# Optimization experiments

Measured on AMD Instinct MI355X. Metric: run time of the kernel, lower is better.

The kernel has to match this reference:

```python
import jax, jax.numpy as jnp
import numpy as np

N = 100000        # total nodes across the batch of graphs
E = 1600000       # directed edges (avg degree 16)
B = 64            # number of graphs
IN_C = 4
HID = 128


def gcn_conv(x, W, b, src, dst, n):
    """PyG GCNConv: add self-loops, symmetric deg normalization, scatter-add."""
    h = x @ W                                   # [n, out]
    loop = jnp.arange(n)
    s = jnp.concatenate([src, loop])            # [E+n] sources (with self-loops)
    d = jnp.concatenate([dst, loop])            # [E+n] targets
    deg = jax.ops.segment_sum(jnp.ones_like(s, dtype=h.dtype), d, num_segments=n)
    dinv = jnp.where(deg > 0, jax.lax.rsqrt(deg), 0.0)
    norm = dinv[s] * dinv[d]                    # [E+n]
    out = jax.ops.segment_sum(h[s] * norm[:, None], d, num_segments=n)
    return out + b


def setup_inputs() -> dict:
    key = jax.random.key(0)
    k1, k2, k3, k4, k5, k6, k7 = jax.random.split(key, 7)
    x = jax.random.normal(k1, (N, IN_C), dtype=jnp.float32)
    edge_index = jax.random.randint(k2, (2, E), 0, N, dtype=jnp.int64)
    batch = jnp.sort(jax.random.randint(k3, (N,), 0, B, dtype=jnp.int64))
    W1 = jax.random.normal(k4, (IN_C, HID), dtype=jnp.float32) / np.sqrt(IN_C)
    b1 = jnp.zeros((HID,), dtype=jnp.float32)
    W2 = jax.random.normal(k5, (HID, HID), dtype=jnp.float32) / np.sqrt(HID)
    b2 = jnp.zeros((HID,), dtype=jnp.float32)
    return {"x": x, "edge_index": edge_index, "batch": batch,
            "W1": W1, "b1": b1, "W2": W2, "b2": b2}


def reference(x, edge_index, batch, W1, b1, W2, b2):
    src, dst = edge_index[0], edge_index[1]
    n = x.shape[0]
    h = jax.nn.relu(gcn_conv(x, W1, b1, src, dst, n))
    h = jax.nn.relu(gcn_conv(h, W2, b2, src, dst, n))
    # global_mean_pool: scatter-mean by graph id
    s = jax.ops.segment_sum(h, batch, num_segments=B)                       # [B, HID]
    cnt = jax.ops.segment_sum(jnp.ones((n,), h.dtype), batch, num_segments=B)
    return s / jnp.maximum(cnt, 1.0)[:, None]
```

## Files before the change

kernel.cpp:

```cpp
#include <hip/hip_runtime.h>

#define TPB 256
#define HID 128
#define IN_C 4
#define SLOT_C 32
#define NB 512
#define EPT 8
#define ECAP 4096
#define OVF_CAP 131072

typedef __attribute__((ext_vector_type(8))) short bf16x8;
typedef __attribute__((ext_vector_type(4))) float f32x4;

union FragU { uint4 u; bf16x8 b; };

__device__ __forceinline__ unsigned f2bf(float f) {
    unsigned u = __float_as_uint(f);
    return (u + 0x7fffu + ((u >> 16) & 1u)) >> 16;
}
__device__ __forceinline__ float bf_lo(unsigned u) { return __uint_as_float(u << 16); }
__device__ __forceinline__ float bf_hi(unsigned u) { return __uint_as_float(u & 0xffff0000u); }

__global__ void k_prep(int* cursor, float* out, int n, int outsz,
                       const float* __restrict__ W2, unsigned short* w2f,
                       const int* __restrict__ batch, int* cnt, int bg,
                       int* ovf_cnt, int* pcur) {
    int nbA = (n + TPB - 1) / TPB;
    int b = blockIdx.x;
    if (b < nbA) {
        int i = b * TPB + threadIdx.x;
        if (i < n) cursor[i] = 0;
        if (i < outsz) out[i] = 0.0f;
    } else if (b < nbA + 64) {
        int i = (b - nbA) * TPB + threadIdx.x;
        if (i < HID * HID) {
            int j = i & 7, frag = i >> 3;
            int lane = frag & 63, blk = frag >> 6;
            int kk = blk >> 3, nt = blk & 7;
            int quad = lane >> 4, nloc = lane & 15;
            int k = kk * 32 + quad * 8 + j;
            int c = nt * 16 + nloc;
            w2f[i] = (unsigned short)f2bf(W2[k * HID + c]);
        }
    } else {
        int g = threadIdx.x;
        if (g == 0) *ovf_cnt = 0;
        for (int z = g; z < NB; z += TPB) pcur[z] = 0;
        if (g < bg) {
            int lo0 = 0, hi0 = n;
            while (lo0 < hi0) { int m = (lo0 + hi0) >> 1; if (batch[m] < g) lo0 = m + 1; else hi0 = m; }
            int lo1 = lo0, hi1 = n;
            while (lo1 < hi1) { int m = (lo1 + hi1) >> 1; if (batch[m] < g + 1) lo1 = m + 1; else hi1 = m; }
            cnt[g] = lo1 - lo0;
        }
    }
}

__global__ __launch_bounds__(256) void k_part(
        const int* __restrict__ src, const int* __restrict__ dst,
        int2* elist, int* pcur, int e, int n) {
    __shared__ int lcnt[2][NB];
    __shared__ int lbase[NB];
    int t = threadIdx.x;
    int c = (t >> 5) & 1;
    for (int z = t; z < NB; z += 256) { lcnt[0][z] = 0; lcnt[1][z] = 0; }
    __syncthreads();

    int base_i = blockIdx.x * (256 * EPT);
    int s[EPT], d[EPT], pr[EPT];
#pragma unroll
    for (int k = 0; k < EPT; k++) {
        int i = base_i + k * 256 + t;
        if (i < e) {
            s[k] = src[i];
            d[k] = dst[i];
            int p = (int)(((long long)d[k] * NB) / n);
            int r = atomicAdd(&lcnt[c][p], 1);
            pr[k] = p | (r << 9);
        } else {
            pr[k] = -1;
        }
    }
    __syncthreads();

    for (int z = t; z < NB; z += 256) {
        int tot = lcnt[0][z] + lcnt[1][z];
        lbase[z] = tot ? atomicAdd(&pcur[z], tot) : 0;
    }
    __syncthreads();

#pragma unroll
    for (int k = 0; k < EPT; k++) {
        if (pr[k] >= 0) {
            int p = pr[k] & (NB - 1);
            int r = pr[k] >> 9;
            int idx = lbase[p] + (c ? lcnt[0][p] : 0) + r;
            if (idx < ECAP)
                elist[(size_t)p * ECAP + idx] = make_int2(s[k], d[k]);
        }
    }
}

__global__ __launch_bounds__(256) void k_build(
        const int2* __restrict__ elist, const int* __restrict__ pcur,
        int* cursor, int* slots, int* ovf, int* ovf_cnt, int n) {
    __shared__ int lcur[512];
    int p = blockIdx.x;
    int t = threadIdx.x;
    int nlo = (int)(((long long)p * n + NB - 1) / NB);
    int nhi = (int)(((long long)(p + 1) * n + NB - 1) / NB);
    int nn = nhi - nlo;
    for (int z = t; z < nn; z += 256) lcur[z] = 0;
    __syncthreads();

    int ne = pcur[p];
    if (ne > ECAP) ne = ECAP;
    for (int j = t; j < ne; j += 256) {
        int2 ed = elist[(size_t)p * ECAP + j];
        int pos = atomicAdd(&lcur[ed.y - nlo], 1);
        if (pos < SLOT_C) {
            slots[ed.y * SLOT_C + pos] = ed.x;
        } else {
            int o = atomicAdd(ovf_cnt, 1);
            if (o < OVF_CAP) {
                ovf[2 * o] = ed.x;
                ovf[2 * o + 1] = ed.y;
            }
        }
    }
    __syncthreads();
    for (int z = t; z < nn; z += 256) cursor[nlo + z] = lcur[z];
}

__global__ void k_dinv(const int* __restrict__ cursor, float* dinv, int n) {
    int i = blockIdx.x * blockDim.x + threadIdx.x;
    if (i < n) dinv[i] = rsqrtf((float)cursor[i] + 1.0f);
}

__global__ __launch_bounds__(256) void k_g1f1(
        const int* __restrict__ cursor, const int* __restrict__ slots,
        const int* __restrict__ ovf, const int* __restrict__ ovf_cnt,
        const float* __restrict__ dinv, const float* __restrict__ x,
        const float* __restrict__ W1, const float* __restrict__ b1,
        unsigned* f1p, int n) {
    __shared__ float xs[256 * 5];
    int t = threadIdx.x;
    int v0 = blockIdx.x * 256;

    int v = v0 + t;
    if (v < n) {
        float dv = dinv[v];
        const float4* x4 = (const float4*)x;
        float4 xv = x4[v];
        float sl = dv * dv;
        float4 A = make_float4(sl * xv.x, sl * xv.y, sl * xv.z, sl * xv.w);
        float4 B = make_float4(0.f, 0.f, 0.f, 0.f);
        float4 C = make_float4(0.f, 0.f, 0.f, 0.f);
        float4 D = make_float4(0.f, 0.f, 0.f, 0.f);
        int deg = cursor[v];
        int m = deg < SLOT_C ? deg : SLOT_C;
        const int* sb = slots + v * SLOT_C;
        int e = 0;
        for (; e + 4 <= m; e += 4) {
            int s0 = sb[e], s1 = sb[e + 1], s2 = sb[e + 2], s3 = sb[e + 3];
            float n0 = dinv[s0] * dv, n1 = dinv[s1] * dv;
            float n2 = dinv[s2] * dv, n3 = dinv[s3] * dv;
            float4 r0 = x4[s0], r1 = x4[s1], r2 = x4[s2], r3 = x4[s3];
            A.x = fmaf(n0, r0.x, A.x); A.y = fmaf(n0, r0.y, A.y);
            A.z = fmaf(n0, r0.z, A.z); A.w = fmaf(n0, r0.w, A.w);
            B.x = fmaf(n1, r1.x, B.x); B.y = fmaf(n1, r1.y, B.y);
            B.z = fmaf(n1, r1.z, B.z); B.w = fmaf(n1, r1.w, B.w);
            C.x = fmaf(n2, r2.x, C.x); C.y = fmaf(n2, r2.y, C.y);
            C.z = fmaf(n2, r2.z, C.z); C.w = fmaf(n2, r2.w, C.w);
            D.x = fmaf(n3, r3.x, D.x); D.y = fmaf(n3, r3.y, D.y);
            D.z = fmaf(n3, r3.z, D.z); D.w = fmaf(n3, r3.w, D.w);
        }
        for (; e < m; e++) {
            int s = sb[e];
            float nm = dinv[s] * dv;
            float4 r = x4[s];
            A.x = fmaf(nm, r.x, A.x); A.y = fmaf(nm, r.y, A.y);
            A.z = fmaf(nm, r.z, A.z); A.w = fmaf(nm, r.w, A.w);
        }
        if (deg > SLOT_C) {
            int oc = *ovf_cnt;
            for (int k = 0; k < oc; k++) {
                if (ovf[2 * k + 1] == v) {
                    int s = ovf[2 * k];
                    float nm = dinv[s] * dv;
                    float4 r = x4[s];
                    A.x = fmaf(nm, r.x, A.x); A.y = fmaf(nm, r.y, A.y);
                    A.z = fmaf(nm, r.z, A.z); A.w = fmaf(nm, r.w, A.w);
                }
            }
        }
        xs[t * 5 + 0] = (A.x + B.x) + (C.x + D.x);
        xs[t * 5 + 1] = (A.y + B.y) + (C.y + D.y);
        xs[t * 5 + 2] = (A.z + B.z) + (C.z + D.z);
        xs[t * 5 + 3] = (A.w + B.w) + (C.w + D.w);
    }
    __syncthreads();

    int cp = t & 63;
    int c0 = cp * 2, c1 = c0 + 1;
    float w00 = W1[c0],           w01 = W1[c1];
    float w10 = W1[HID + c0],     w11 = W1[HID + c1];
    float w20 = W1[2 * HID + c0], w21 = W1[2 * HID + c1];
    float w30 = W1[3 * HID + c0], w31 = W1[3 * HID + c1];
    float bb0 = b1[c0],           bb1 = b1[c1];
    int g = t >> 6;
    for (int iter = 0; iter < 64; iter++) {
        int node = iter * 4 + g;
        int vv = v0 + node;
        if (vv >= n) break;
        float x0 = xs[node * 5 + 0], x1 = xs[node * 5 + 1];
        float x2 = xs[node * 5 + 2], x3 = xs[node * 5 + 3];
        float s0 = fmaf(x0, w00, fmaf(x1, w10, fmaf(x2, w20, fmaf(x3, w30, bb0))));
        float s1 = fmaf(x0, w01, fmaf(x1, w11, fmaf(x2, w21, fmaf(x3, w31, bb1))));
        s0 = s0 > 0.0f ? s0 : 0.0f;
        s1 = s1 > 0.0f ? s1 : 0.0f;
        f1p[(size_t)vv * 64 + cp] = f2bf(s0) | (f2bf(s1) << 16);
    }
}

__global__ __launch_bounds__(256) void k_gather2(
        const int* __restrict__ cursor, const int* __restrict__ slots,
        const int* __restrict__ ovf, const int* __restrict__ ovf_cnt,
        const float* __restrict__ dinv, const unsigned* __restrict__ f1p,
        unsigned* acc2b, int n) {
    int wv = threadIdx.x >> 6;
    int ln = threadIdx.x & 63;
    int h  = ln >> 5;
    int q  = ln & 31;
    int v = blockIdx.x * 4 + wv;
    if (v >= n) return;
    float dv = dinv[v];
    const uint2* F = (const uint2*)f1p;

    uint2 us = F[(size_t)v * 32 + q];
    float sl = (h == 0) ? dv * dv : 0.0f;
    float A[4] = { sl * bf_lo(us.x), sl * bf_hi(us.x),
                   sl * bf_lo(us.y), sl * bf_hi(us.y) };
    float B[4] = {0.f, 0.f, 0.f, 0.f};
    float C[4] = {0.f, 0.f, 0.f, 0.f};
    float D[4] = {0.f, 0.f, 0.f, 0.f};

    int deg = cursor[v];
    int m = deg < SLOT_C ? deg : SLOT_C;
    const int* sb = slots + v * SLOT_C;
    int e = 0;
    for (; e + 8 <= m; e += 8) {
        int sA = sb[e + h];
        int sB = sb[e + 2 + h];
        int sC = sb[e + 4 + h];
        int sD = sb[e + 6 + h];
        float nA = dinv[sA] * dv, nB = dinv[sB] * dv;
        float nC = dinv[sC] * dv, nD = dinv[sD] * dv;
        uint2 uA = F[(size_t)sA * 32 + q];
        uint2 uB = F[(size_t)sB * 32 + q];
        uint2 uC = F[(size_t)sC * 32 + q];
        uint2 uD = F[(size_t)sD * 32 + q];
        A[0] = fmaf(nA, bf_lo(uA.x), A[0]); A[1] = fmaf(nA, bf_hi(uA.x), A[1]);
        A[2] = fmaf(nA, bf_lo(uA.y), A[2]); A[3] = fmaf(nA, bf_hi(uA.y), A[3]);
        B[0] = fmaf(nB, bf_lo(uB.x), B[0]); B[1] = fmaf(nB, bf_hi(uB.x), B[1]);
        B[2] = fmaf(nB, bf_lo(uB.y), B[2]); B[3] = fmaf(nB, bf_hi(uB.y), B[3]);
        C[0] = fmaf(nC, bf_lo(uC.x), C[0]); C[1] = fmaf(nC, bf_hi(uC.x), C[1]);
        C[2] = fmaf(nC, bf_lo(uC.y), C[2]); C[3] = fmaf(nC, bf_hi(uC.y), C[3]);
        D[0] = fmaf(nD, bf_lo(uD.x), D[0]); D[1] = fmaf(nD, bf_hi(uD.x), D[1]);
        D[2] = fmaf(nD, bf_lo(uD.y), D[2]); D[3] = fmaf(nD, bf_hi(uD.y), D[3]);
    }
    for (; e + 2 <= m; e += 2) {
        int s = sb[e + h];
        float nm = dinv[s] * dv;
        uint2 u = F[(size_t)s * 32 + q];
        A[0] = fmaf(nm, bf_lo(u.x), A[0]); A[1] = fmaf(nm, bf_hi(u.x), A[1]);
        A[2] = fmaf(nm, bf_lo(u.y), A[2]); A[3] = fmaf(nm, bf_hi(u.y), A[3]);
    }
    if (e < m) {
        int s = sb[e];
        float nm = (h == 0) ? dinv[s] * dv : 0.0f;
        uint2 u = F[(size_t)s * 32 + q];
        A[0] = fmaf(nm, bf_lo(u.x), A[0]); A[1] = fmaf(nm, bf_hi(u.x), A[1]);
        A[2] = fmaf(nm, bf_lo(u.y), A[2]); A[3] = fmaf(nm, bf_hi(u.y), A[3]);
    }
    if (deg > SLOT_C) {
        int oc = *ovf_cnt;
        for (int k = 0; k < oc; k++) {
            if (ovf[2 * k + 1] == v && h == 0) {
                int s = ovf[2 * k];
                float nm = dinv[s] * dv;
                uint2 u = F[(size_t)s * 32 + q];
                A[0] = fmaf(nm, bf_lo(u.x), A[0]); A[1] = fmaf(nm, bf_hi(u.x), A[1]);
                A[2] = fmaf(nm, bf_lo(u.y), A[2]); A[3] = fmaf(nm, bf_hi(u.y), A[3]);
            }
        }
    }

    float o0 = (A[0] + B[0]) + (C[0] + D[0]);
    float o1 = (A[1] + B[1]) + (C[1] + D[1]);
    float o2 = (A[2] + B[2]) + (C[2] + D[2]);
    float o3 = (A[3] + B[3]) + (C[3] + D[3]);
    o0 += __shfl_xor(o0, 32, 64);
    o1 += __shfl_xor(o1, 32, 64);
    o2 += __shfl_xor(o2, 32, 64);
    o3 += __shfl_xor(o3, 32, 64);
    if (h == 0) {
        uint2 w;
        w.x = f2bf(o0) | (f2bf(o1) << 16);
        w.y = f2bf(o2) | (f2bf(o3) << 16);
        ((uint2*)acc2b)[(size_t)v * 32 + q] = w;
    }
}

__global__ __launch_bounds__(256) void k_mm2_pool(
        const unsigned* __restrict__ acc2b, const unsigned short* __restrict__ w2f,
        const float* __restrict__ b2, const int* __restrict__ batch,
        float* out, int n) {
    __shared__ int bch[64];
    int t = threadIdx.x;
    int w = t >> 6, lane = t & 63;
    int quad = lane >> 4, nloc = lane & 15;
    int v0 = blockIdx.x * 64;
    if (t < 64) {
        int v = v0 + t;
        bch[t] = (v < n) ? batch[v] : -1;
    }
    __syncthreads();

    int va = v0 + w * 16 + nloc;
    if (va >= n) va = n - 1;

    const uint4* A4 = (const uint4*)acc2b;
    const uint4* B4 = (const uint4*)w2f;

    f32x4 acc[8];
#pragma unroll
    for (int nt = 0; nt < 8; nt++) acc[nt] = (f32x4){0.f, 0.f, 0.f, 0.f};

#pragma unroll
    for (int kk = 0; kk < 4; kk++) {
        FragU af;
        af.u = A4[(size_t)va * 16 + kk * 4 + quad];
#pragma unroll
        for (int nt = 0; nt < 8; nt++) {
            FragU bf;
            bf.u = B4[(kk * 8 + nt) * 64 + lane];
            acc[nt] = __builtin_amdgcn_mfma_f32_16x16x32_bf16(af.b, bf.b, acc[nt], 0, 0, 0);
        }
    }

    int b0 = bch[w * 16], b15 = bch[w * 16 + 15];
    if (b0 == b15 && b0 >= 0) {
#pragma unroll
        for (int nt = 0; nt < 8; nt++) {
            float bias = b2[nt * 16 + nloc];
            float s = 0.f;
#pragma unroll
            for (int reg = 0; reg < 4; reg++) {
                float f = acc[nt][reg] + bias;
                s += f > 0.f ? f : 0.f;
            }
            s += __shfl_xor(s, 16, 64);
            s += __shfl_xor(s, 32, 64);
            if (lane < 16) atomicAdd(&out[b0 * HID + nt * 16 + lane], s);
        }
    } else {
#pragma unroll
        for (int nt = 0; nt < 8; nt++) {
            float bias = b2[nt * 16 + nloc];
            int cur = -1; float run = 0.f;
#pragma unroll
            for (int reg = 0; reg < 4; reg++) {
                int b = bch[w * 16 + quad * 4 + reg];
                if (b < 0) continue;
                float f = acc[nt][reg] + bias;
                f = f > 0.f ? f : 0.f;
                if (b != cur) {
                    if (cur >= 0) atomicAdd(&out[cur * HID + nt * 16 + nloc], run);
                    run = 0.f; cur = b;
                }
                run += f;
            }
            if (cur >= 0) atomicAdd(&out[cur * HID + nt * 16 + nloc], run);
        }
    }
}

__global__ void k_div(float* out, const int* __restrict__ cnt, int outsz) {
    int i = blockIdx.x * blockDim.x + threadIdx.x;
    if (i < outsz) {
        int b = i >> 7;
        float cf = (float)cnt[b];
        out[i] = out[i] / fmaxf(cf, 1.0f);
    }
}

extern "C" void kernel_launch(void* const* d_in, const int* in_sizes, int n_in,
                              void* d_out, int out_size, void* d_ws, size_t ws_size,
                              hipStream_t stream) {
    const float* x   = (const float*)d_in[0];
    const int* ei    = (const int*)d_in[1];
    const int* batch = (const int*)d_in[2];
    const float* W1  = (const float*)d_in[3];
    const float* b1  = (const float*)d_in[4];
    const float* W2  = (const float*)d_in[5];
    const float* b2  = (const float*)d_in[6];
    float* out = (float*)d_out;

    int n  = in_sizes[0] / IN_C;
    int e  = in_sizes[1] / 2;
    int bg = out_size / HID;
    const int* src = ei;
    const int* dst = ei + e;

    size_t off_b = 0;
    char* base = (char*)d_ws;
    auto carve = [&](size_t bytes) -> void* {
        void* p = base + off_b;
        off_b += (bytes + 255) & ~(size_t)255;
        return p;
    };
    int*            cursor  = (int*)carve((size_t)n * 4);
    int*            slots   = (int*)carve((size_t)n * SLOT_C * 4);
    int*            ovf     = (int*)carve((size_t)OVF_CAP * 2 * 4);
    int*            ovf_cnt = (int*)carve(256);
    int*            pcur    = (int*)carve((size_t)NB * 4);
    int2*           elist   = (int2*)carve((size_t)NB * ECAP * 8);
    float*          dinv    = (float*)carve((size_t)n * 4);
    unsigned*       f1p     = (unsigned*)carve((size_t)n * 64 * 4);
    unsigned*       acc2b   = (unsigned*)carve((size_t)n * 64 * 4);
    unsigned short* w2f     = (unsigned short*)carve((size_t)HID * HID * 2);
    int*            cnt     = (int*)carve((size_t)bg * 4);
    (void)ws_size;

    int gN = (n + TPB - 1) / TPB;
    int gP = (e + 256 * EPT - 1) / (256 * EPT);

    k_prep<<<gN + 64 + 1, TPB, 0, stream>>>(cursor, out, n, out_size, W2, w2f,
                                            batch, cnt, bg, ovf_cnt, pcur);
    k_part<<<gP, TPB, 0, stream>>>(src, dst, elist, pcur, e, n);
    k_build<<<NB, TPB, 0, stream>>>(elist, pcur, cursor, slots, ovf, ovf_cnt, n);
    k_dinv<<<gN, TPB, 0, stream>>>(cursor, dinv, n);
    k_g1f1<<<gN, TPB, 0, stream>>>(cursor, slots, ovf, ovf_cnt, dinv, x, W1, b1, f1p, n);
    k_gather2<<<(n + 3) / 4, 256, 0, stream>>>(cursor, slots, ovf, ovf_cnt, dinv, f1p, acc2b, n);
    k_mm2_pool<<<(n + 63) / 64, 256, 0, stream>>>(acc2b, w2f, b2, batch, out, n);
    k_div<<<(out_size + TPB - 1) / TPB, TPB, 0, stream>>>(out, cnt, out_size);
}
```

Baseline: 249.8 us.

## Split layer-1 features into channel slabs and gather per slab

Layer-1 output features are now stored as 8 channel slabs of 16 bf16 channels (32 bytes per node per slab) instead of one 256-byte row per node. The second-layer gather runs one block per 64 nodes per slab, so each slab's working set (about 3.2 MB) can stay in cache while random neighbor rows are fetched. Within a wave, 16 edge groups of 4 lanes each handle a node's edges in parallel and are reduced with shuffles. The cost is that slots, dinv and cursor are read 8 times, and the 32-byte random reads are narrower per request.

```diff
diff --git a/kernel.cpp b/kernel.cpp
--- a/kernel.cpp
+++ b/kernel.cpp
@@ -208,6 +208,7 @@
     float w20 = W1[2 * HID + c0], w21 = W1[2 * HID + c1];
     float w30 = W1[3 * HID + c0], w31 = W1[3 * HID + c1];
     float bb0 = b1[c0],           bb1 = b1[c1];
+    size_t sb_off = (size_t)(cp >> 3) * (size_t)n * 8 + (cp & 7);
     int g = t >> 6;
     for (int iter = 0; iter < 64; iter++) {
         int node = iter * 4 + g;
@@ -219,96 +220,70 @@
         float s1 = fmaf(x0, w01, fmaf(x1, w11, fmaf(x2, w21, fmaf(x3, w31, bb1))));
         s0 = s0 > 0.0f ? s0 : 0.0f;
         s1 = s1 > 0.0f ? s1 : 0.0f;
-        f1p[(size_t)vv * 64 + cp] = f2bf(s0) | (f2bf(s1) << 16);
-    }
-}
-
-__global__ __launch_bounds__(256) void k_gather2(
+        f1p[sb_off + (size_t)vv * 8] = f2bf(s0) | (f2bf(s1) << 16);
+    }
+}
+
+__global__ __launch_bounds__(256) void k_gather2s(
         const int* __restrict__ cursor, const int* __restrict__ slots,
         const int* __restrict__ ovf, const int* __restrict__ ovf_cnt,
-        const float* __restrict__ dinv, const unsigned* __restrict__ f1p,
+        const float* __restrict__ dinv, const unsigned* __restrict__ f1ps,
         unsigned* acc2b, int n) {
+    int cs = blockIdx.x & 7;
+    int blkn = blockIdx.x >> 3;
     int wv = threadIdx.x >> 6;
     int ln = threadIdx.x & 63;
-    int h  = ln >> 5;
-    int q  = ln & 31;
-    int v = blockIdx.x * 4 + wv;
-    if (v >= n) return;
-    float dv = dinv[v];
-    const uint2* F = (const uint2*)f1p;
-
-    uint2 us = F[(size_t)v * 32 + q];
-    float sl = (h == 0) ? dv * dv : 0.0f;
-    float A[4] = { sl * bf_lo(us.x), sl * bf_hi(us.x),
-                   sl * bf_lo(us.y), sl * bf_hi(us.y) };
-    float B[4] = {0.f, 0.f, 0.f, 0.f};
-    float C[4] = {0.f, 0.f, 0.f, 0.f};
-    float D[4] = {0.f, 0.f, 0.f, 0.f};
-
-    int deg = cursor[v];
-    int m = deg < SLOT_C ? deg : SLOT_C;
-    const int* sb = slots + v * SLOT_C;
-    int e = 0;
-    for (; e + 8 <= m; e += 8) {
-        int sA = sb[e + h];
-        int sB = sb[e + 2 + h];
-        int sC = sb[e + 4 + h];
-        int sD = sb[e + 6 + h];
-        float nA = dinv[sA] * dv, nB = dinv[sB] * dv;
-        float nC = dinv[sC] * dv, nD = dinv[sD] * dv;
-        uint2 uA = F[(size_t)sA * 32 + q];
-        uint2 uB = F[(size_t)sB * 32 + q];
-        uint2 uC = F[(size_t)sC * 32 + q];
-        uint2 uD = F[(size_t)sD * 32 + q];
-        A[0] = fmaf(nA, bf_lo(uA.x), A[0]); A[1] = fmaf(nA, bf_hi(uA.x), A[1]);
-        A[2] = fmaf(nA, bf_lo(uA.y), A[2]); A[3] = fmaf(nA, bf_hi(uA.y), A[3]);
-        B[0] = fmaf(nB, bf_lo(uB.x), B[0]); B[1] = fmaf(nB, bf_hi(uB.x), B[1]);
-        B[2] = fmaf(nB, bf_lo(uB.y), B[2]); B[3] = fmaf(nB, bf_hi(uB.y), B[3]);
-        C[0] = fmaf(nC, bf_lo(uC.x), C[0]); C[1] = fmaf(nC, bf_hi(uC.x), C[1]);
-        C[2] = fmaf(nC, bf_lo(uC.y), C[2]); C[3] = fmaf(nC, bf_hi(uC.y), C[3]);
-        D[0] = fmaf(nD, bf_lo(uD.x), D[0]); D[1] = fmaf(nD, bf_hi(uD.x), D[1]);
-        D[2] = fmaf(nD, bf_lo(uD.y), D[2]); D[3] = fmaf(nD, bf_hi(uD.y), D[3]);
-    }
-    for (; e + 2 <= m; e += 2) {
-        int s = sb[e + h];
-        float nm = dinv[s] * dv;
-        uint2 u = F[(size_t)s * 32 + q];
-        A[0] = fmaf(nm, bf_lo(u.x), A[0]); A[1] = fmaf(nm, bf_hi(u.x), A[1]);
-        A[2] = fmaf(nm, bf_lo(u.y), A[2]); A[3] = fmaf(nm, bf_hi(u.y), A[3]);
-    }
-    if (e < m) {
-        int s = sb[e];
-        float nm = (h == 0) ? dinv[s] * dv : 0.0f;
-        uint2 u = F[(size_t)s * 32 + q];
-        A[0] = fmaf(nm, bf_lo(u.x), A[0]); A[1] = fmaf(nm, bf_hi(u.x), A[1]);
-        A[2] = fmaf(nm, bf_lo(u.y), A[2]); A[3] = fmaf(nm, bf_hi(u.y), A[3]);
-    }
-    if (deg > SLOT_C) {
-        int oc = *ovf_cnt;
-        for (int k = 0; k < oc; k++) {
-            if (ovf[2 * k + 1] == v && h == 0) {
-                int s = ovf[2 * k];
-                float nm = dinv[s] * dv;
-                uint2 u = F[(size_t)s * 32 + q];
-                A[0] = fmaf(nm, bf_lo(u.x), A[0]); A[1] = fmaf(nm, bf_hi(u.x), A[1]);
-                A[2] = fmaf(nm, bf_lo(u.y), A[2]); A[3] = fmaf(nm, bf_hi(u.y), A[3]);
+    int eg = ln >> 2;
+    int wd2 = ln & 3;
+    const uint2* F2 = (const uint2*)(f1ps + (size_t)cs * (size_t)n * 8);
+    int vb = blkn * 64 + wv * 16;
+    for (int nd = 0; nd < 16; nd++) {
+        int v = vb + nd;
+        if (v >= n) break;
+        float dv = dinv[v];
+        int deg = cursor[v];
+        int m = deg < SLOT_C ? deg : SLOT_C;
+        const int* sb = slots + v * SLOT_C;
+        float a0, a1, a2, a3;
+        if (eg == 0) {
+            uint2 u = F2[(size_t)v * 4 + wd2];
+            float sl = dv * dv;
+            a0 = sl * bf_lo(u.x); a1 = sl * bf_hi(u.x);
+            a2 = sl * bf_lo(u.y); a3 = sl * bf_hi(u.y);
+        } else { a0 = 0.f; a1 = 0.f; a2 = 0.f; a3 = 0.f; }
+        for (int e = eg; e < m; e += 16) {
+            int s = sb[e];
+            float nm = dinv[s] * dv;
+            uint2 u = F2[(size_t)s * 4 + wd2];
+            a0 = fmaf(nm, bf_lo(u.x), a0); a1 = fmaf(nm, bf_hi(u.x), a1);
+            a2 = fmaf(nm, bf_lo(u.y), a2); a3 = fmaf(nm, bf_hi(u.y), a3);
+        }
+        if (deg > SLOT_C && eg == 0) {
+            int oc = *ovf_cnt;
+            for (int k = 0; k < oc; k++) {
+                if (ovf[2 * k + 1] == v) {
+                    int s = ovf[2 * k];
+                    float nm = dinv[s] * dv;
+                    uint2 u = F2[(size_t)s * 4 + wd2];
+                    a0 = fmaf(nm, bf_lo(u.x), a0); a1 = fmaf(nm, bf_hi(u.x), a1);
+                    a2 = fmaf(nm, bf_lo(u.y), a2); a3 = fmaf(nm, bf_hi(u.y), a3);
+                }
             }
         }
-    }
-
-    float o0 = (A[0] + B[0]) + (C[0] + D[0]);
-    float o1 = (A[1] + B[1]) + (C[1] + D[1]);
-    float o2 = (A[2] + B[2]) + (C[2] + D[2]);
-    float o3 = (A[3] + B[3]) + (C[3] + D[3]);
-    o0 += __shfl_xor(o0, 32, 64);
-    o1 += __shfl_xor(o1, 32, 64);
-    o2 += __shfl_xor(o2, 32, 64);
-    o3 += __shfl_xor(o3, 32, 64);
-    if (h == 0) {
-        uint2 w;
-        w.x = f2bf(o0) | (f2bf(o1) << 16);
-        w.y = f2bf(o2) | (f2bf(o3) << 16);
-        ((uint2*)acc2b)[(size_t)v * 32 + q] = w;
+        a0 += __shfl_xor(a0, 4, 64);  a1 += __shfl_xor(a1, 4, 64);
+        a2 += __shfl_xor(a2, 4, 64);  a3 += __shfl_xor(a3, 4, 64);
+        a0 += __shfl_xor(a0, 8, 64);  a1 += __shfl_xor(a1, 8, 64);
+        a2 += __shfl_xor(a2, 8, 64);  a3 += __shfl_xor(a3, 8, 64);
+        a0 += __shfl_xor(a0, 16, 64); a1 += __shfl_xor(a1, 16, 64);
+        a2 += __shfl_xor(a2, 16, 64); a3 += __shfl_xor(a3, 16, 64);
+        a0 += __shfl_xor(a0, 32, 64); a1 += __shfl_xor(a1, 32, 64);
+        a2 += __shfl_xor(a2, 32, 64); a3 += __shfl_xor(a3, 32, 64);
+        if (eg == 0) {
+            uint2 w;
+            w.x = f2bf(a0) | (f2bf(a1) << 16);
+            w.y = f2bf(a2) | (f2bf(a3) << 16);
+            ((uint2*)acc2b)[(size_t)v * 32 + cs * 4 + wd2] = w;
+        }
     }
 }
 
@@ -435,6 +410,7 @@
 
     int gN = (n + TPB - 1) / TPB;
     int gP = (e + 256 * EPT - 1) / (256 * EPT);
+    int gS = ((n + 63) / 64) * 8;
 
     k_prep<<<gN + 64 + 1, TPB, 0, stream>>>(cursor, out, n, out_size, W2, w2f,
                                             batch, cnt, bg, ovf_cnt, pcur);
@@ -442,7 +418,7 @@
     k_build<<<NB, TPB, 0, stream>>>(elist, pcur, cursor, slots, ovf, ovf_cnt, n);
     k_dinv<<<gN, TPB, 0, stream>>>(cursor, dinv, n);
     k_g1f1<<<gN, TPB, 0, stream>>>(cursor, slots, ovf, ovf_cnt, dinv, x, W1, b1, f1p, n);
-    k_gather2<<<(n + 3) / 4, 256, 0, stream>>>(cursor, slots, ovf, ovf_cnt, dinv, f1p, acc2b, n);
+    k_gather2s<<<gS, 256, 0, stream>>>(cursor, slots, ovf, ovf_cnt, dinv, f1p, acc2b, n);
     k_mm2_pool<<<(n + 63) / 64, 256, 0, stream>>>(acc2b, w2f, b2, batch, out, n);
     k_div<<<(out_size + TPB - 1) / TPB, TPB, 0, stream>>>(out, cnt, out_size);
 }
```

After: 405.3 us. 1.62x slower.
